# Optimization experiments

Hardware: AMD Instinct MI355X
Metric: run time of the kernel (lower is better)

The kernel has to match this reference:

```python
import jax, jax.numpy as jnp
import numpy as np


def setup_inputs() -> dict:
    key = jax.random.key(0)
    ks = jax.random.split(key, 9)
    B, T, S, E, H = 4, 4096, 4096, 512, 64
    return {
        "x": jax.random.normal(ks[0], (B, T, 1), dtype=jnp.float32),
        "tok_emb": jax.random.normal(ks[1], (B, S, E), dtype=jnp.float32),
        "key_w": jax.random.normal(ks[2], (H, E), dtype=jnp.float32) * 0.05,
        "key_b": jax.random.normal(ks[3], (H,), dtype=jnp.float32) * 0.05,
        "query_w": jax.random.normal(ks[4], (H, 1), dtype=jnp.float32) * 0.05,
        "query_b": jax.random.normal(ks[5], (H,), dtype=jnp.float32) * 0.05,
        "value_w": jax.random.normal(ks[6], (H, E), dtype=jnp.float32) * 0.05,
        "proj_w": jax.random.normal(ks[7], (1, H), dtype=jnp.float32) * 0.05,
        "proj_b": jax.random.normal(ks[8], (1,), dtype=jnp.float32) * 0.05,
    }


def reference(x, tok_emb, key_w, key_b, query_w, query_b, value_w, proj_w, proj_b):
    # k = tanh(Linear(tok_emb))            [B,S,H]
    k = jnp.tanh(jnp.einsum("bse,he->bsh", tok_emb, key_w) + key_b)
    # q = tanh(Linear(x)); x last dim is 1 [B,T,H]
    q = jnp.tanh(jnp.einsum("btu,hu->bth", x, query_w) + query_b)
    scale = k.shape[-1] ** (-0.5)
    wei = jnp.einsum("bth,bsh->bts", q, k) * scale  # [B,T,S]
    # NOTE: softmax over dim=-2 (the query/T axis), faithful to the original
    wei = jax.nn.softmax(wei, axis=-2)
    v = jnp.tanh(jnp.einsum("bse,he->bsh", tok_emb, value_w))  # [B,S,H]
    out = jnp.tanh(jnp.einsum("bts,bsh->bth", wei, v))         # [B,T,H]
    out = jnp.einsum("bth,oh->bto", out, proj_w) + proj_b      # [B,T,1]
    return jnp.squeeze(out, axis=-1)                            # [B,T]
```

## Files before the change

### kernel.cpp

```cpp
#include <hip/hip_runtime.h>
#include <math.h>

#define BB 4
#define TT 4096
#define SS 4096
#define EE 512
#define HH 64
#define NN 128
#define XR 6.0f


typedef __attribute__((ext_vector_type(8))) __bf16 bf16x8;
typedef __attribute__((ext_vector_type(16))) float f32x16;

__device__ __forceinline__ unsigned short f2b(float f) {
  unsigned int u = __float_as_uint(f);
  return (unsigned short)((u + 0x7FFFu + ((u >> 16) & 1u)) >> 16);
}

__global__ __launch_bounds__(256) void prep_sm_kernel(
    const float* __restrict__ kw, const float* __restrict__ vw,
    const float* __restrict__ qw, const float* __restrict__ qb,
    const float* __restrict__ x, unsigned int* __restrict__ Wfrag,
    float* __restrict__ Cmat, unsigned short* __restrict__ qnA,
    float* __restrict__ Sm_part) {
  const int blk = blockIdx.x;
  if (blk < 64) {
    int idx = blk * 256 + threadIdx.x;
    int jq = idx & 1;
    int l = (idx >> 1) & 63;
    int ks = (idx >> 7) & 31;
    int nb = idx >> 12;
    int n = nb * 32 + (l & 31);
    int k = ks * 16 + (l >> 5) * 8 + jq * 4;
    const float* row = (n < HH) ? (kw + n * EE + k) : (vw + (n - HH) * EE + k);
    float4 wv = *(const float4*)row;
    Wfrag[idx * 2] = (unsigned int)f2b(wv.x) | ((unsigned int)f2b(wv.y) << 16);
    Wfrag[idx * 2 + 1] =
        (unsigned int)f2b(wv.z) | ((unsigned int)f2b(wv.w) << 16);
  } else if (blk < 128) {
    int idx = (blk - 64) * 256 + threadIdx.x;
    int m = idx >> 7;
    int j = idx & (NN - 1);
    Cmat[idx] = (float)cos((double)m * (M_PI * (j + 0.5) / NN));
  } else if (blk < 160) {
    int idx = (blk - 128) * 256 + threadIdx.x;
    int h = idx & 63;
    int j = idx >> 6;
    double th = M_PI * (j + 0.5) / NN;
    float xj = (float)(XR * cos(th));
    float val = tanhf(fmaf(xj, qw[h], qb[h]));
    int pos = (((j >> 5) * 4 + (h >> 4)) * 64 + (j & 31) + 32 * ((h >> 3) & 1)) * 8 +
              (h & 7);
    qnA[pos] = f2b(val);
  } else {
    __shared__ float theta[128];
    int blk2 = blk - 160;
    int b = blk2 >> 5;
    int chunk = blk2 & 31;
    int t0 = chunk * 128;
    int tid = threadIdx.x;
    if (tid < 128) {
      float xh = x[b * TT + t0 + tid] * (1.0f / XR);
      xh = fminf(1.0f, fmaxf(-1.0f, xh));
      theta[tid] = acosf(xh);
    }
    __syncthreads();
    if (tid < 128) {
      float m = (float)tid;
      float acc = 0.f;
#pragma unroll 8
      for (int i = 0; i < 128; ++i) acc += cosf(m * theta[i]);
      Sm_part[(b * 32 + chunk) * NN + tid] = acc;
    }
  }
}

__global__ __launch_bounds__(256) void kvattn_kernel(
    const float* __restrict__ emb, const float* __restrict__ kb,
    const unsigned int* __restrict__ Wfrag, const unsigned short* __restrict__ qnA,
    const float* __restrict__ Cmat, const float* __restrict__ Sm_part,
    float* __restrict__ Opart) {
  __shared__ __align__(16) char smem[69120];
  unsigned short* A_lds = (unsigned short*)smem;
  unsigned short* ktB = (unsigned short*)smem;
  unsigned short* vB = (unsigned short*)(smem + 8192);
  unsigned short* eA = (unsigned short*)(smem + 16384);
  float* zred = (float*)(smem + 65536);
  float* wql = (float*)(smem + 67840);
  float* izl = (float*)(smem + 68352);
  float* sml = (float*)(smem + 68608);

  const int tid = threadIdx.x;
  const int row0 = blockIdx.x * 64;
  const int bb = row0 >> 12;
  const int sc = (row0 >> 6) & 63;

#pragma unroll
  for (int mb = 0; mb < 2; ++mb) {
    int m = tid >> 3;
    int c8 = tid & 7;
    const float* src = emb + (size_t)(row0 + mb * 32 + m) * EE;
    unsigned short* dst = A_lds + mb * 16384;
#pragma unroll
    for (int it = 0; it < 16; ++it) {
      int k = (c8 + it * 8) * 4;
      float4 v = *(const float4*)(src + k);
      int kstep = k >> 4;
      int lane = m + 32 * ((k >> 3) & 1);
      int j = k & 7;
      unsigned int lo = (unsigned int)f2b(v.x) | ((unsigned int)f2b(v.y) << 16);
      unsigned int hi = (unsigned int)f2b(v.z) | ((unsigned int)f2b(v.w) << 16);
      *(uint2*)&dst[(kstep * 64 + lane) * 8 + j] = make_uint2(lo, hi);
    }
  }
  if (tid < 128) {
    float s = 0.f;
#pragma unroll 8
    for (int c = 0; c < 32; ++c) s += Sm_part[(bb * 32 + c) * NN + tid];
    sml[tid] = s;
  }
  __syncthreads();
  if (tid < 128) {
    float acc = sml[0] * (1.0f / NN);
    for (int m = 1; m < NN; ++m)
      acc = fmaf(sml[m] * (2.0f / NN), Cmat[m * NN + tid], acc);
    wql[tid] = acc;
  }

  const int w = tid >> 6;
  const int lane = tid & 63;
  f32x16 acc0 = {}, acc1 = {};
  const bf16x8* Bf = (const bf16x8*)Wfrag;
#pragma unroll 4
  for (int kstep = 0; kstep < 32; ++kstep) {
    bf16x8 bfr = Bf[(w * 32 + kstep) * 64 + lane];
    bf16x8 a0 = *(const bf16x8*)&A_lds[(kstep * 64 + lane) * 8];
    bf16x8 a1 = *(const bf16x8*)&A_lds[16384 + (kstep * 64 + lane) * 8];
    acc0 = __builtin_amdgcn_mfma_f32_32x32x16_bf16(a0, bfr, acc0, 0, 0, 0);
    acc1 = __builtin_amdgcn_mfma_f32_32x32x16_bf16(a1, bfr, acc1, 0, 0, 0);
  }
  __syncthreads();

  {
    const int n = w * 32 + (lane & 31);
    if (w < 2) {
      float kbv = kb[n];
      const int ks_h = n >> 4;
      const int off_h = 32 * ((n >> 3) & 1);
      const int jj_h = n & 7;
#pragma unroll
      for (int reg = 0; reg < 16; ++reg) {
        int sl = (reg & 3) + 8 * (reg >> 2) + 4 * (lane >> 5);
        ktB[(ks_h * 64 + sl + off_h) * 8 + jj_h] = f2b(tanhf(acc0[reg] + kbv));
        ktB[((4 + ks_h) * 64 + sl + off_h) * 8 + jj_h] =
            f2b(tanhf(acc1[reg] + kbv));
      }
    } else {
      int h = n - 64;
      const int nb_h = h >> 5;
      const int lm = h & 31;
#pragma unroll
      for (int reg = 0; reg < 16; ++reg) {
        int sl = (reg & 3) + 8 * (reg >> 2) + 4 * (lane >> 5);
        int s1 = sl + 32;
        vB[((nb_h * 4 + (sl >> 4)) * 64 + lm + 32 * ((sl >> 3) & 1)) * 8 +
           (sl & 7)] = f2b(tanhf(acc0[reg]));
        vB[((nb_h * 4 + (s1 >> 4)) * 64 + lm + 32 * ((s1 >> 3) & 1)) * 8 +
           (s1 & 7)] = f2b(tanhf(acc1[reg]));
      }
    }
  }
  __syncthreads();

  f32x16 l0 = {}, l1 = {};
#pragma unroll
  for (int ks = 0; ks < 4; ++ks) {
    bf16x8 a = *(const bf16x8*)(qnA + ((w * 4 + ks) * 64 + lane) * 8);
    bf16x8 b0 = *(const bf16x8*)&ktB[(ks * 64 + lane) * 8];
    bf16x8 b1 = *(const bf16x8*)&ktB[((4 + ks) * 64 + lane) * 8];
    l0 = __builtin_amdgcn_mfma_f32_32x32x16_bf16(a, b0, l0, 0, 0, 0);
    l1 = __builtin_amdgcn_mfma_f32_32x32x16_bf16(a, b1, l1, 0, 0, 0);
  }
  float e0[16], e1[16];
  float zp0 = 0.f, zp1 = 0.f;
#pragma unroll
  for (int r = 0; r < 4; ++r) {
    float4 wq4 = *(const float4*)&wql[w * 32 + 8 * r + 4 * (lane >> 5)];
    float wa[4] = {wq4.x, wq4.y, wq4.z, wq4.w};
#pragma unroll
    for (int c = 0; c < 4; ++c) {
      int reg = 4 * r + c;
      e0[reg] = __expf(l0[reg] * 0.125f);
      e1[reg] = __expf(l1[reg] * 0.125f);
      zp0 = fmaf(wa[c], e0[reg], zp0);
      zp1 = fmaf(wa[c], e1[reg], zp1);
    }
  }
  zred[(lane & 31) * 9 + w * 2 + (lane >> 5)] = zp0;
  zred[(32 + (lane & 31)) * 9 + w * 2 + (lane >> 5)] = zp1;
  __syncthreads();
  if (tid < 64) {
    float sum = 0.f;
#pragma unroll
    for (int k = 0; k < 8; ++k) sum += zred[tid * 9 + k];
    izl[tid] = 1.0f / sum;
  }
  __syncthreads();

  {
    const int sA = lane & 31, sB = 32 + (lane & 31);
    const float izA = izl[sA], izB = izl[sB];
    const int ksA = sA >> 4, oA = 32 * ((sA >> 3) & 1), jA = sA & 7;
    const int ksB = sB >> 4, oB = 32 * ((sB >> 3) & 1), jB = sB & 7;
#pragma unroll
    for (int reg = 0; reg < 16; ++reg) {
      int jl = (reg & 3) + 8 * (reg >> 2) + 4 * (lane >> 5);
      eA[((w * 4 + ksA) * 64 + jl + oA) * 8 + jA] = f2b(e0[reg] * izA);
      eA[((w * 4 + ksB) * 64 + jl + oB) * 8 + jB] = f2b(e1[reg] * izB);
    }
  }
  __syncthreads();
  f32x16 o0 = {}, o1 = {};
#pragma unroll
  for (int ks = 0; ks < 4; ++ks) {
    bf16x8 a = *(const bf16x8*)&eA[((w * 4 + ks) * 64 + lane) * 8];
    bf16x8 b0 = *(const bf16x8*)&vB[(ks * 64 + lane) * 8];
    bf16x8 b1 = *(const bf16x8*)&vB[((4 + ks) * 64 + lane) * 8];
    o0 = __builtin_amdgcn_mfma_f32_32x32x16_bf16(a, b0, o0, 0, 0, 0);
    o1 = __builtin_amdgcn_mfma_f32_32x32x16_bf16(a, b1, o1, 0, 0, 0);
  }
  float* op = Opart + (size_t)(bb * 64 + sc) * (NN * HH);
  const int h0 = lane & 31, h1 = 32 + (lane & 31);
#pragma unroll
  for (int reg = 0; reg < 16; ++reg) {
    int j = w * 32 + (reg & 3) + 8 * (reg >> 2) + 4 * (lane >> 5);
    op[j * HH + h0] = o0[reg];
    op[j * HH + h1] = o1[reg];
  }
}

__global__ __launch_bounds__(256) void oy_kernel(const float* __restrict__ Opart,
                                                 const float* __restrict__ pw,
                                                 const float* __restrict__ pb,
                                                 float* __restrict__ ynode) {
  __shared__ float part[2][4][64];
  const int tid = threadIdx.x;
  const int b = blockIdx.x >> 6;
  const int j0 = (blockIdx.x & 63) * 2;
  const int h = tid & 63;
  const int q = tid >> 6;
#pragma unroll
  for (int jj = 0; jj < 2; ++jj) {
    float s = 0.f;
#pragma unroll
    for (int i = 0; i < 16; ++i)
      s += Opart[((size_t)(b * 64 + q * 16 + i) * NN + j0 + jj) * HH + h];
    part[jj][q][h] = s;
  }
  __syncthreads();
  if (tid < 128) {
    int jj = tid >> 6;
    int lane = tid & 63;
    float o = part[jj][0][lane] + part[jj][1][lane] + part[jj][2][lane] +
              part[jj][3][lane];
    float v = tanhf(o) * pw[lane];
#pragma unroll
    for (int off = 32; off > 0; off >>= 1) v += __shfl_down(v, off, 64);
    if (lane == 0) ynode[b * NN + j0 + jj] = v + pb[0];
  }
}

__global__ __launch_bounds__(256) void final_kernel(
    const float* __restrict__ x, const float* __restrict__ ynode,
    const float* __restrict__ Cmat, float* __restrict__ y) {
  const int idx = blockIdx.x * 256 + threadIdx.x;
  const int b = idx >> 12;
  __shared__ float yl[NN];
  __shared__ float c[NN];
  if (threadIdx.x < NN) yl[threadIdx.x] = ynode[b * NN + threadIdx.x];
  __syncthreads();
  if (threadIdx.x < NN) {
    int m = threadIdx.x;
    double acc = 0.0;
#pragma unroll 8
    for (int j = 0; j < NN; ++j)
      acc += (double)yl[j] * (double)Cmat[m * NN + j];
    c[m] = (float)(acc * ((m == 0 ? 1.0 : 2.0) / NN));
  }
  __syncthreads();
  float xf = x[idx] * (1.0f / XR);
  xf = fminf(1.0f, fmaxf(-1.0f, xf));
  double xh = (double)xf;
  double b1 = 0.0, b2 = 0.0;
  for (int m = NN - 1; m >= 1; --m) {
    double t = fma(2.0 * xh, b1, (double)c[m] - b2);
    b2 = b1;
    b1 = t;
  }
  y[idx] = (float)fma(xh, b1, (double)c[0] - b2);
}

extern "C" void kernel_launch(void* const* d_in, const int* in_sizes, int n_in,
                              void* d_out, int out_size, void* d_ws,
                              size_t ws_size, hipStream_t stream) {
  const float* x = (const float*)d_in[0];
  const float* emb = (const float*)d_in[1];
  const float* kw = (const float*)d_in[2];
  const float* kb = (const float*)d_in[3];
  const float* qw = (const float*)d_in[4];
  const float* qb = (const float*)d_in[5];
  const float* vw = (const float*)d_in[6];
  const float* pw = (const float*)d_in[7];
  const float* pb = (const float*)d_in[8];

  float* ws = (float*)d_ws;
  float* Opart = ws;
  float* Cmat = ws + (2 << 20);
  unsigned short* qnA = (unsigned short*)(Cmat + 16384);
  unsigned int* Wfrag = (unsigned int*)(Cmat + 16384 + 4096);
  float* Sm_part = (float*)(Wfrag + 32768);
  float* ynode = Sm_part + 16384;
  float* y = (float*)d_out;

  prep_sm_kernel<<<288, 256, 0, stream>>>(kw, vw, qw, qb, x, Wfrag, Cmat, qnA,
                                          Sm_part);
  kvattn_kernel<<<BB * SS / 64, 256, 0, stream>>>(emb, kb, Wfrag, qnA, Cmat,
                                                  Sm_part, Opart);
  oy_kernel<<<BB * NN / 2, 256, 0, stream>>>(Opart, pw, pb, ynode);
  final_kernel<<<BB * TT / 256, 256, 0, stream>>>(x, ynode, Cmat, y);
}
```

Baseline: 135.3 us.

## Fuse four kernels into one cooperative kernel with grid-wide syncs

Merges the prep, KV-attention, output reduction and final Chebyshev evaluation kernels into a single cooperative launch of 256 blocks separated by grid.sync barriers. This removes three kernel launch boundaries and their idle gaps. The prep work is redistributed across the 256 blocks, and the final stage now uses only 64 of 256 threads per block. Grid barriers have their own cost, and the cooperative launch requires all 256 blocks with 69KB of shared memory each to be resident at once.

```diff
diff --git a/kernel.cpp b/kernel.cpp
--- a/kernel.cpp
+++ b/kernel.cpp
@@ -1,5 +1,8 @@
 #include <hip/hip_runtime.h>
+#include <hip/hip_cooperative_groups.h>
 #include <math.h>
+
+namespace cg = cooperative_groups;
 
 #define BB 4
 #define TT 4096
@@ -18,15 +21,48 @@
   return (unsigned short)((u + 0x7FFFu + ((u >> 16) & 1u)) >> 16);
 }
 
-__global__ __launch_bounds__(256) void prep_sm_kernel(
-    const float* __restrict__ kw, const float* __restrict__ vw,
+__global__ __launch_bounds__(256) void mega_kernel(
+    const float* __restrict__ x, const float* __restrict__ emb,
+    const float* __restrict__ kw, const float* __restrict__ kb,
     const float* __restrict__ qw, const float* __restrict__ qb,
-    const float* __restrict__ x, unsigned int* __restrict__ Wfrag,
+    const float* __restrict__ vw, const float* __restrict__ pw,
+    const float* __restrict__ pb, unsigned int* __restrict__ Wfrag,
     float* __restrict__ Cmat, unsigned short* __restrict__ qnA,
-    float* __restrict__ Sm_part) {
+    float* __restrict__ Sm_part, float* __restrict__ Opart,
+    float* __restrict__ ynode, float* __restrict__ y) {
+  cg::grid_group grid = cg::this_grid();
+  __shared__ __align__(16) char smem[69120];
+  const int tid = threadIdx.x;
   const int blk = blockIdx.x;
-  if (blk < 64) {
-    int idx = blk * 256 + threadIdx.x;
+
+  if (blk < 128) {
+    float* theta = (float*)(smem + 65536);
+    int b = blk >> 5, chunk = blk & 31, t0 = chunk * 128;
+    if (tid < 128) {
+      float xh = x[b * TT + t0 + tid] * (1.0f / XR);
+      xh = fminf(1.0f, fmaxf(-1.0f, xh));
+      theta[tid] = acosf(xh);
+    }
+    __syncthreads();
+    if (tid < 128) {
+      float m = (float)tid;
+      float acc = 0.f;
+#pragma unroll 8
+      for (int i = 0; i < 128; ++i) acc += cosf(m * theta[i]);
+      Sm_part[(b * 32 + chunk) * NN + tid] = acc;
+    }
+  } else if (blk < 160) {
+    int idx = (blk - 128) * 256 + tid;
+    int h = idx & 63;
+    int j = idx >> 6;
+    double th = M_PI * (j + 0.5) / NN;
+    float xj = (float)(XR * cos(th));
+    float val = tanhf(fmaf(xj, qw[h], qb[h]));
+    int pos = (((j >> 5) * 4 + (h >> 4)) * 64 + (j & 31) + 32 * ((h >> 3) & 1)) * 8 +
+              (h & 7);
+    qnA[pos] = f2b(val);
+  } else if (blk < 224) {
+    int idx = (blk - 160) * 256 + tid;
     int jq = idx & 1;
     int l = (idx >> 1) & 63;
     int ks = (idx >> 7) & 31;
@@ -38,267 +74,237 @@
     Wfrag[idx * 2] = (unsigned int)f2b(wv.x) | ((unsigned int)f2b(wv.y) << 16);
     Wfrag[idx * 2 + 1] =
         (unsigned int)f2b(wv.z) | ((unsigned int)f2b(wv.w) << 16);
-  } else if (blk < 128) {
-    int idx = (blk - 64) * 256 + threadIdx.x;
-    int m = idx >> 7;
-    int j = idx & (NN - 1);
-    Cmat[idx] = (float)cos((double)m * (M_PI * (j + 0.5) / NN));
-  } else if (blk < 160) {
-    int idx = (blk - 128) * 256 + threadIdx.x;
-    int h = idx & 63;
-    int j = idx >> 6;
-    double th = M_PI * (j + 0.5) / NN;
-    float xj = (float)(XR * cos(th));
-    float val = tanhf(fmaf(xj, qw[h], qb[h]));
-    int pos = (((j >> 5) * 4 + (h >> 4)) * 64 + (j & 31) + 32 * ((h >> 3) & 1)) * 8 +
-              (h & 7);
-    qnA[pos] = f2b(val);
   } else {
-    __shared__ float theta[128];
-    int blk2 = blk - 160;
-    int b = blk2 >> 5;
-    int chunk = blk2 & 31;
-    int t0 = chunk * 128;
-    int tid = threadIdx.x;
-    if (tid < 128) {
-      float xh = x[b * TT + t0 + tid] * (1.0f / XR);
-      xh = fminf(1.0f, fmaxf(-1.0f, xh));
-      theta[tid] = acosf(xh);
-    }
-    __syncthreads();
-    if (tid < 128) {
-      float m = (float)tid;
-      float acc = 0.f;
+    int idx = (blk - 224) * 256 + tid;
+#pragma unroll
+    for (int r = 0; r < 2; ++r) {
+      int id2 = idx + r * 8192;
+      int m = id2 >> 7;
+      int j = id2 & (NN - 1);
+      Cmat[id2] = (float)cos((double)m * (M_PI * (j + 0.5) / NN));
+    }
+  }
+  grid.sync();
+
+  {
+    unsigned short* A_lds = (unsigned short*)smem;
+    unsigned short* ktB = (unsigned short*)smem;
+    unsigned short* vB = (unsigned short*)(smem + 8192);
+    unsigned short* eA = (unsigned short*)(smem + 16384);
+    float* zred = (float*)(smem + 65536);
+    float* wql = (float*)(smem + 67840);
+    float* izl = (float*)(smem + 68352);
+    float* sml = (float*)(smem + 68608);
+
+    const int row0 = blk * 64;
+    const int bb = row0 >> 12;
+    const int sc = (row0 >> 6) & 63;
+
+#pragma unroll
+    for (int mb = 0; mb < 2; ++mb) {
+      int m = tid >> 3;
+      int c8 = tid & 7;
+      const float* src = emb + (size_t)(row0 + mb * 32 + m) * EE;
+      unsigned short* dst = A_lds + mb * 16384;
+#pragma unroll
+      for (int it = 0; it < 16; ++it) {
+        int k = (c8 + it * 8) * 4;
+        float4 v = *(const float4*)(src + k);
+        int kstep = k >> 4;
+        int lane = m + 32 * ((k >> 3) & 1);
+        int j = k & 7;
+        unsigned int lo =
+            (unsigned int)f2b(v.x) | ((unsigned int)f2b(v.y) << 16);
+        unsigned int hi =
+            (unsigned int)f2b(v.z) | ((unsigned int)f2b(v.w) << 16);
+        *(uint2*)&dst[(kstep * 64 + lane) * 8 + j] = make_uint2(lo, hi);
+      }
+    }
+    if (tid < 128) {
+      float s = 0.f;
 #pragma unroll 8
-      for (int i = 0; i < 128; ++i) acc += cosf(m * theta[i]);
-      Sm_part[(b * 32 + chunk) * NN + tid] = acc;
+      for (int c = 0; c < 32; ++c) s += Sm_part[(bb * 32 + c) * NN + tid];
+      sml[tid] = s;
+    }
+    __syncthreads();
+    if (tid < 128) {
+      float acc = sml[0] * (1.0f / NN);
+      for (int m = 1; m < NN; ++m)
+        acc = fmaf(sml[m] * (2.0f / NN), Cmat[m * NN + tid], acc);
+      wql[tid] = acc;
+    }
+
+    const int w = tid >> 6;
+    const int lane = tid & 63;
+    f32x16 acc0 = {}, acc1 = {};
+    const bf16x8* Bf = (const bf16x8*)Wfrag;
+#pragma unroll 4
+    for (int kstep = 0; kstep < 32; ++kstep) {
+      bf16x8 bfr = Bf[(w * 32 + kstep) * 64 + lane];
+      bf16x8 a0 = *(const bf16x8*)&A_lds[(kstep * 64 + lane) * 8];
+      bf16x8 a1 = *(const bf16x8*)&A_lds[16384 + (kstep * 64 + lane) * 8];
+      acc0 = __builtin_amdgcn_mfma_f32_32x32x16_bf16(a0, bfr, acc0, 0, 0, 0);
+      acc1 = __builtin_amdgcn_mfma_f32_32x32x16_bf16(a1, bfr, acc1, 0, 0, 0);
+    }
+    __syncthreads();
+
+    {
+      const int n = w * 32 + (lane & 31);
+      if (w < 2) {
+        float kbv = kb[n];
+        const int ks_h = n >> 4;
+        const int off_h = 32 * ((n >> 3) & 1);
+        const int jj_h = n & 7;
+#pragma unroll
+        for (int reg = 0; reg < 16; ++reg) {
+          int sl = (reg & 3) + 8 * (reg >> 2) + 4 * (lane >> 5);
+          ktB[(ks_h * 64 + sl + off_h) * 8 + jj_h] =
+              f2b(tanhf(acc0[reg] + kbv));
+          ktB[((4 + ks_h) * 64 + sl + off_h) * 8 + jj_h] =
+              f2b(tanhf(acc1[reg] + kbv));
+        }
+      } else {
+        int h = n - 64;
+        const int nb_h = h >> 5;
+        const int lm = h & 31;
+#pragma unroll
+        for (int reg = 0; reg < 16; ++reg) {
+          int sl = (reg & 3) + 8 * (reg >> 2) + 4 * (lane >> 5);
+          int s1 = sl + 32;
+          vB[((nb_h * 4 + (sl >> 4)) * 64 + lm + 32 * ((sl >> 3) & 1)) * 8 +
+             (sl & 7)] = f2b(tanhf(acc0[reg]));
+          vB[((nb_h * 4 + (s1 >> 4)) * 64 + lm + 32 * ((s1 >> 3) & 1)) * 8 +
+             (s1 & 7)] = f2b(tanhf(acc1[reg]));
+        }
+      }
+    }
+    __syncthreads();
+
+    f32x16 l0 = {}, l1 = {};
+#pragma unroll
+    for (int ks = 0; ks < 4; ++ks) {
+      bf16x8 a = *(const bf16x8*)(qnA + ((w * 4 + ks) * 64 + lane) * 8);
+      bf16x8 b0 = *(const bf16x8*)&ktB[(ks * 64 + lane) * 8];
+      bf16x8 b1 = *(const bf16x8*)&ktB[((4 + ks) * 64 + lane) * 8];
+      l0 = __builtin_amdgcn_mfma_f32_32x32x16_bf16(a, b0, l0, 0, 0, 0);
+      l1 = __builtin_amdgcn_mfma_f32_32x32x16_bf16(a, b1, l1, 0, 0, 0);
+    }
+    float e0[16], e1[16];
+    float zp0 = 0.f, zp1 = 0.f;
+#pragma unroll
+    for (int r = 0; r < 4; ++r) {
+      float4 wq4 = *(const float4*)&wql[w * 32 + 8 * r + 4 * (lane >> 5)];
+      float wa[4] = {wq4.x, wq4.y, wq4.z, wq4.w};
+#pragma unroll
+      for (int c = 0; c < 4; ++c) {
+        int reg = 4 * r + c;
+        e0[reg] = __expf(l0[reg] * 0.125f);
+        e1[reg] = __expf(l1[reg] * 0.125f);
+        zp0 = fmaf(wa[c], e0[reg], zp0);
+        zp1 = fmaf(wa[c], e1[reg], zp1);
+      }
+    }
+    zred[(lane & 31) * 9 + w * 2 + (lane >> 5)] = zp0;
+    zred[(32 + (lane & 31)) * 9 + w * 2 + (lane >> 5)] = zp1;
+    __syncthreads();
+    if (tid < 64) {
+      float sum = 0.f;
+#pragma unroll
+      for (int k = 0; k < 8; ++k) sum += zred[tid * 9 + k];
+      izl[tid] = 1.0f / sum;
+    }
+    __syncthreads();
+
+    {
+      const int sA = lane & 31, sB = 32 + (lane & 31);
+      const float izA = izl[sA], izB = izl[sB];
+      const int ksA = sA >> 4, oA = 32 * ((sA >> 3) & 1), jA = sA & 7;
+      const int ksB = sB >> 4, oB = 32 * ((sB >> 3) & 1), jB = sB & 7;
+#pragma unroll
+      for (int reg = 0; reg < 16; ++reg) {
+        int jl = (reg & 3) + 8 * (reg >> 2) + 4 * (lane >> 5);
+        eA[((w * 4 + ksA) * 64 + jl + oA) * 8 + jA] = f2b(e0[reg] * izA);
+        eA[((w * 4 + ksB) * 64 + jl + oB) * 8 + jB] = f2b(e1[reg] * izB);
+      }
+    }
+    __syncthreads();
+    f32x16 o0 = {}, o1 = {};
+#pragma unroll
+    for (int ks = 0; ks < 4; ++ks) {
+      bf16x8 a = *(const bf16x8*)&eA[((w * 4 + ks) * 64 + lane) * 8];
+      bf16x8 b0 = *(const bf16x8*)&vB[(ks * 64 + lane) * 8];
+      bf16x8 b1 = *(const bf16x8*)&vB[((4 + ks) * 64 + lane) * 8];
+      o0 = __builtin_amdgcn_mfma_f32_32x32x16_bf16(a, b0, o0, 0, 0, 0);
+      o1 = __builtin_amdgcn_mfma_f32_32x32x16_bf16(a, b1, o1, 0, 0, 0);
+    }
+    float* op = Opart + (size_t)(bb * 64 + sc) * (NN * HH);
+    const int h0 = lane & 31, h1 = 32 + (lane & 31);
+#pragma unroll
+    for (int reg = 0; reg < 16; ++reg) {
+      int j = w * 32 + (reg & 3) + 8 * (reg >> 2) + 4 * (lane >> 5);
+      op[j * HH + h0] = o0[reg];
+      op[j * HH + h1] = o1[reg];
     }
   }
-}
-
-__global__ __launch_bounds__(256) void kvattn_kernel(
-    const float* __restrict__ emb, const float* __restrict__ kb,
-    const unsigned int* __restrict__ Wfrag, const unsigned short* __restrict__ qnA,
-    const float* __restrict__ Cmat, const float* __restrict__ Sm_part,
-    float* __restrict__ Opart) {
-  __shared__ __align__(16) char smem[69120];
-  unsigned short* A_lds = (unsigned short*)smem;
-  unsigned short* ktB = (unsigned short*)smem;
-  unsigned short* vB = (unsigned short*)(smem + 8192);
-  unsigned short* eA = (unsigned short*)(smem + 16384);
-  float* zred = (float*)(smem + 65536);
-  float* wql = (float*)(smem + 67840);
-  float* izl = (float*)(smem + 68352);
-  float* sml = (float*)(smem + 68608);
-
-  const int tid = threadIdx.x;
-  const int row0 = blockIdx.x * 64;
-  const int bb = row0 >> 12;
-  const int sc = (row0 >> 6) & 63;
-
-#pragma unroll
-  for (int mb = 0; mb < 2; ++mb) {
-    int m = tid >> 3;
-    int c8 = tid & 7;
-    const float* src = emb + (size_t)(row0 + mb * 32 + m) * EE;
-    unsigned short* dst = A_lds + mb * 16384;
-#pragma unroll
-    for (int it = 0; it < 16; ++it) {
-      int k = (c8 + it * 8) * 4;
-      float4 v = *(const float4*)(src + k);
-      int kstep = k >> 4;
-      int lane = m + 32 * ((k >> 3) & 1);
-      int j = k & 7;
-      unsigned int lo = (unsigned int)f2b(v.x) | ((unsigned int)f2b(v.y) << 16);
-      unsigned int hi = (unsigned int)f2b(v.z) | ((unsigned int)f2b(v.w) << 16);
-      *(uint2*)&dst[(kstep * 64 + lane) * 8 + j] = make_uint2(lo, hi);
+  grid.sync();
+
+  {
+    float (*part)[4][64] = (float(*)[4][64])smem;
+    const int b = blk >> 6;
+    const int j0 = (blk & 63) * 2;
+    const int h = tid & 63;
+    const int q = tid >> 6;
+#pragma unroll
+    for (int jj = 0; jj < 2; ++jj) {
+      float s = 0.f;
+#pragma unroll
+      for (int i = 0; i < 16; ++i)
+        s += Opart[((size_t)(b * 64 + q * 16 + i) * NN + j0 + jj) * HH + h];
+      part[jj][q][h] = s;
+    }
+    __syncthreads();
+    if (tid < 128) {
+      int jj = tid >> 6;
+      int lane = tid & 63;
+      float o = part[jj][0][lane] + part[jj][1][lane] + part[jj][2][lane] +
+                part[jj][3][lane];
+      float v = tanhf(o) * pw[lane];
+#pragma unroll
+      for (int off = 32; off > 0; off >>= 1) v += __shfl_down(v, off, 64);
+      if (lane == 0) ynode[b * NN + j0 + jj] = v + pb[0];
     }
   }
-  if (tid < 128) {
-    float s = 0.f;
+  grid.sync();
+
+  {
+    float* yl = (float*)smem;
+    float* c = (float*)(smem + 512);
+    const int base = blk * 64;
+    const int b = base >> 12;
+    if (tid < NN) yl[tid] = ynode[b * NN + tid];
+    __syncthreads();
+    if (tid < NN) {
+      double acc = 0.0;
 #pragma unroll 8
-    for (int c = 0; c < 32; ++c) s += Sm_part[(bb * 32 + c) * NN + tid];
-    sml[tid] = s;
+      for (int j = 0; j < NN; ++j)
+        acc += (double)yl[j] * (double)Cmat[tid * NN + j];
+      c[tid] = (float)(acc * ((tid == 0 ? 1.0 : 2.0) / NN));
+    }
+    __syncthreads();
+    if (tid < 64) {
+      const int idx = base + tid;
+      float xf = x[idx] * (1.0f / XR);
+      xf = fminf(1.0f, fmaxf(-1.0f, xf));
+      double xh = (double)xf;
+      double b1 = 0.0, b2 = 0.0;
+      for (int m = NN - 1; m >= 1; --m) {
+        double t = fma(2.0 * xh, b1, (double)c[m] - b2);
+        b2 = b1;
+        b1 = t;
+      }
+      y[idx] = (float)fma(xh, b1, (double)c[0] - b2);
+    }
   }
-  __syncthreads();
-  if (tid < 128) {
-    float acc = sml[0] * (1.0f / NN);
-    for (int m = 1; m < NN; ++m)
-      acc = fmaf(sml[m] * (2.0f / NN), Cmat[m * NN + tid], acc);
-    wql[tid] = acc;
-  }
-
-  const int w = tid >> 6;
-  const int lane = tid & 63;
-  f32x16 acc0 = {}, acc1 = {};
-  const bf16x8* Bf = (const bf16x8*)Wfrag;
-#pragma unroll 4
-  for (int kstep = 0; kstep < 32; ++kstep) {
-    bf16x8 bfr = Bf[(w * 32 + kstep) * 64 + lane];
-    bf16x8 a0 = *(const bf16x8*)&A_lds[(kstep * 64 + lane) * 8];
-    bf16x8 a1 = *(const bf16x8*)&A_lds[16384 + (kstep * 64 + lane) * 8];
-    acc0 = __builtin_amdgcn_mfma_f32_32x32x16_bf16(a0, bfr, acc0, 0, 0, 0);
-    acc1 = __builtin_amdgcn_mfma_f32_32x32x16_bf16(a1, bfr, acc1, 0, 0, 0);
-  }
-  __syncthreads();
-
-  {
-    const int n = w * 32 + (lane & 31);
-    if (w < 2) {
-      float kbv = kb[n];
-      const int ks_h = n >> 4;
-      const int off_h = 32 * ((n >> 3) & 1);
-      const int jj_h = n & 7;
-#pragma unroll
-      for (int reg = 0; reg < 16; ++reg) {
-        int sl = (reg & 3) + 8 * (reg >> 2) + 4 * (lane >> 5);
-        ktB[(ks_h * 64 + sl + off_h) * 8 + jj_h] = f2b(tanhf(acc0[reg] + kbv));
-        ktB[((4 + ks_h) * 64 + sl + off_h) * 8 + jj_h] =
-            f2b(tanhf(acc1[reg] + kbv));
-      }
-    } else {
-      int h = n - 64;
-      const int nb_h = h >> 5;
-      const int lm = h & 31;
-#pragma unroll
-      for (int reg = 0; reg < 16; ++reg) {
-        int sl = (reg & 3) + 8 * (reg >> 2) + 4 * (lane >> 5);
-        int s1 = sl + 32;
-        vB[((nb_h * 4 + (sl >> 4)) * 64 + lm + 32 * ((sl >> 3) & 1)) * 8 +
-           (sl & 7)] = f2b(tanhf(acc0[reg]));
-        vB[((nb_h * 4 + (s1 >> 4)) * 64 + lm + 32 * ((s1 >> 3) & 1)) * 8 +
-           (s1 & 7)] = f2b(tanhf(acc1[reg]));
-      }
-    }
-  }
-  __syncthreads();
-
-  f32x16 l0 = {}, l1 = {};
-#pragma unroll
-  for (int ks = 0; ks < 4; ++ks) {
-    bf16x8 a = *(const bf16x8*)(qnA + ((w * 4 + ks) * 64 + lane) * 8);
-    bf16x8 b0 = *(const bf16x8*)&ktB[(ks * 64 + lane) * 8];
-    bf16x8 b1 = *(const bf16x8*)&ktB[((4 + ks) * 64 + lane) * 8];
-    l0 = __builtin_amdgcn_mfma_f32_32x32x16_bf16(a, b0, l0, 0, 0, 0);
-    l1 = __builtin_amdgcn_mfma_f32_32x32x16_bf16(a, b1, l1, 0, 0, 0);
-  }
-  float e0[16], e1[16];
-  float zp0 = 0.f, zp1 = 0.f;
-#pragma unroll
-  for (int r = 0; r < 4; ++r) {
-    float4 wq4 = *(const float4*)&wql[w * 32 + 8 * r + 4 * (lane >> 5)];
-    float wa[4] = {wq4.x, wq4.y, wq4.z, wq4.w};
-#pragma unroll
-    for (int c = 0; c < 4; ++c) {
-      int reg = 4 * r + c;
-      e0[reg] = __expf(l0[reg] * 0.125f);
-      e1[reg] = __expf(l1[reg] * 0.125f);
-      zp0 = fmaf(wa[c], e0[reg], zp0);
-      zp1 = fmaf(wa[c], e1[reg], zp1);
-    }
-  }
-  zred[(lane & 31) * 9 + w * 2 + (lane >> 5)] = zp0;
-  zred[(32 + (lane & 31)) * 9 + w * 2 + (lane >> 5)] = zp1;
-  __syncthreads();
-  if (tid < 64) {
-    float sum = 0.f;
-#pragma unroll
-    for (int k = 0; k < 8; ++k) sum += zred[tid * 9 + k];
-    izl[tid] = 1.0f / sum;
-  }
-  __syncthreads();
-
-  {
-    const int sA = lane & 31, sB = 32 + (lane & 31);
-    const float izA = izl[sA], izB = izl[sB];
-    const int ksA = sA >> 4, oA = 32 * ((sA >> 3) & 1), jA = sA & 7;
-    const int ksB = sB >> 4, oB = 32 * ((sB >> 3) & 1), jB = sB & 7;
-#pragma unroll
-    for (int reg = 0; reg < 16; ++reg) {
-      int jl = (reg & 3) + 8 * (reg >> 2) + 4 * (lane >> 5);
-      eA[((w * 4 + ksA) * 64 + jl + oA) * 8 + jA] = f2b(e0[reg] * izA);
-      eA[((w * 4 + ksB) * 64 + jl + oB) * 8 + jB] = f2b(e1[reg] * izB);
-    }
-  }
-  __syncthreads();
-  f32x16 o0 = {}, o1 = {};
-#pragma unroll
-  for (int ks = 0; ks < 4; ++ks) {
-    bf16x8 a = *(const bf16x8*)&eA[((w * 4 + ks) * 64 + lane) * 8];
-    bf16x8 b0 = *(const bf16x8*)&vB[(ks * 64 + lane) * 8];
-    bf16x8 b1 = *(const bf16x8*)&vB[((4 + ks) * 64 + lane) * 8];
-    o0 = __builtin_amdgcn_mfma_f32_32x32x16_bf16(a, b0, o0, 0, 0, 0);
-    o1 = __builtin_amdgcn_mfma_f32_32x32x16_bf16(a, b1, o1, 0, 0, 0);
-  }
-  float* op = Opart + (size_t)(bb * 64 + sc) * (NN * HH);
-  const int h0 = lane & 31, h1 = 32 + (lane & 31);
-#pragma unroll
-  for (int reg = 0; reg < 16; ++reg) {
-    int j = w * 32 + (reg & 3) + 8 * (reg >> 2) + 4 * (lane >> 5);
-    op[j * HH + h0] = o0[reg];
-    op[j * HH + h1] = o1[reg];
-  }
-}
-
-__global__ __launch_bounds__(256) void oy_kernel(const float* __restrict__ Opart,
-                                                 const float* __restrict__ pw,
-                                                 const float* __restrict__ pb,
-                                                 float* __restrict__ ynode) {
-  __shared__ float part[2][4][64];
-  const int tid = threadIdx.x;
-  const int b = blockIdx.x >> 6;
-  const int j0 = (blockIdx.x & 63) * 2;
-  const int h = tid & 63;
-  const int q = tid >> 6;
-#pragma unroll
-  for (int jj = 0; jj < 2; ++jj) {
-    float s = 0.f;
-#pragma unroll
-    for (int i = 0; i < 16; ++i)
-      s += Opart[((size_t)(b * 64 + q * 16 + i) * NN + j0 + jj) * HH + h];
-    part[jj][q][h] = s;
-  }
-  __syncthreads();
-  if (tid < 128) {
-    int jj = tid >> 6;
-    int lane = tid & 63;
-    float o = part[jj][0][lane] + part[jj][1][lane] + part[jj][2][lane] +
-              part[jj][3][lane];
-    float v = tanhf(o) * pw[lane];
-#pragma unroll
-    for (int off = 32; off > 0; off >>= 1) v += __shfl_down(v, off, 64);
-    if (lane == 0) ynode[b * NN + j0 + jj] = v + pb[0];
-  }
-}
-
-__global__ __launch_bounds__(256) void final_kernel(
-    const float* __restrict__ x, const float* __restrict__ ynode,
-    const float* __restrict__ Cmat, float* __restrict__ y) {
-  const int idx = blockIdx.x * 256 + threadIdx.x;
-  const int b = idx >> 12;
-  __shared__ float yl[NN];
-  __shared__ float c[NN];
-  if (threadIdx.x < NN) yl[threadIdx.x] = ynode[b * NN + threadIdx.x];
-  __syncthreads();
-  if (threadIdx.x < NN) {
-    int m = threadIdx.x;
-    double acc = 0.0;
-#pragma unroll 8
-    for (int j = 0; j < NN; ++j)
-      acc += (double)yl[j] * (double)Cmat[m * NN + j];
-    c[m] = (float)(acc * ((m == 0 ? 1.0 : 2.0) / NN));
-  }
-  __syncthreads();
-  float xf = x[idx] * (1.0f / XR);
-  xf = fminf(1.0f, fmaxf(-1.0f, xf));
-  double xh = (double)xf;
-  double b1 = 0.0, b2 = 0.0;
-  for (int m = NN - 1; m >= 1; --m) {
-    double t = fma(2.0 * xh, b1, (double)c[m] - b2);
-    b2 = b1;
-    b1 = t;
-  }
-  y[idx] = (float)fma(xh, b1, (double)c[0] - b2);
 }
 
 extern "C" void kernel_launch(void* const* d_in, const int* in_sizes, int n_in,
@@ -323,10 +329,9 @@
   float* ynode = Sm_part + 16384;
   float* y = (float*)d_out;
 
-  prep_sm_kernel<<<288, 256, 0, stream>>>(kw, vw, qw, qb, x, Wfrag, Cmat, qnA,
-                                          Sm_part);
-  kvattn_kernel<<<BB * SS / 64, 256, 0, stream>>>(emb, kb, Wfrag, qnA, Cmat,
-                                                  Sm_part, Opart);
-  oy_kernel<<<BB * NN / 2, 256, 0, stream>>>(Opart, pw, pb, ynode);
-  final_kernel<<<BB * TT / 256, 256, 0, stream>>>(x, ynode, Cmat, y);
+  void* args[] = {&x,  &emb,   &kw,   &kb,      &qw,    &qb,
+                  &vw, &pw,    &pb,   &Wfrag,   &Cmat,  &qnA,
+                  &Sm_part, &Opart, &ynode, &y};
+  hipLaunchCooperativeKernel((void*)mega_kernel, dim3(256), dim3(256), args, 0,
+                             stream);
 }
```

Result: slower. 230.1 us (+70.1%).

## Stage embedding tile in two halves to halve LDS footprint

Applied to the files above, without the earlier changes.

The 64-row embedding tile is now converted to bf16 and staged in LDS one 32-row half at a time, with the MFMA loop split into two passes that reuse a single 32 KB buffer. This cuts the kernel's shared memory from about 69 KB to about 36 KB so more blocks can be resident per CU. In exchange the Wfrag fragments are loaded twice, extra barriers are added, and the second half's global load is serialized behind the first half's compute within a block.

```diff
diff --git a/kernel.cpp b/kernel.cpp
--- a/kernel.cpp
+++ b/kernel.cpp
@@ -81,37 +81,38 @@
     const unsigned int* __restrict__ Wfrag, const unsigned short* __restrict__ qnA,
     const float* __restrict__ Cmat, const float* __restrict__ Sm_part,
     float* __restrict__ Opart) {
-  __shared__ __align__(16) char smem[69120];
-  unsigned short* A_lds = (unsigned short*)smem;
+  __shared__ __align__(16) char smem[36352];
+  unsigned short* A_half = (unsigned short*)smem;
   unsigned short* ktB = (unsigned short*)smem;
   unsigned short* vB = (unsigned short*)(smem + 8192);
   unsigned short* eA = (unsigned short*)(smem + 16384);
-  float* zred = (float*)(smem + 65536);
-  float* wql = (float*)(smem + 67840);
-  float* izl = (float*)(smem + 68352);
-  float* sml = (float*)(smem + 68608);
+  float* zred = (float*)(smem + 32768);
+  float* wql = (float*)(smem + 35072);
+  float* izl = (float*)(smem + 35584);
+  float* sml = (float*)(smem + 35840);
 
   const int tid = threadIdx.x;
   const int row0 = blockIdx.x * 64;
   const int bb = row0 >> 12;
   const int sc = (row0 >> 6) & 63;
-
-#pragma unroll
-  for (int mb = 0; mb < 2; ++mb) {
+  const int w = tid >> 6;
+  const int lane = tid & 63;
+  const bf16x8* Bf = (const bf16x8*)Wfrag;
+
+  {
     int m = tid >> 3;
     int c8 = tid & 7;
-    const float* src = emb + (size_t)(row0 + mb * 32 + m) * EE;
-    unsigned short* dst = A_lds + mb * 16384;
+    const float* src = emb + (size_t)(row0 + m) * EE;
 #pragma unroll
     for (int it = 0; it < 16; ++it) {
       int k = (c8 + it * 8) * 4;
       float4 v = *(const float4*)(src + k);
       int kstep = k >> 4;
-      int lane = m + 32 * ((k >> 3) & 1);
+      int l = m + 32 * ((k >> 3) & 1);
       int j = k & 7;
       unsigned int lo = (unsigned int)f2b(v.x) | ((unsigned int)f2b(v.y) << 16);
       unsigned int hi = (unsigned int)f2b(v.z) | ((unsigned int)f2b(v.w) << 16);
-      *(uint2*)&dst[(kstep * 64 + lane) * 8 + j] = make_uint2(lo, hi);
+      *(uint2*)&A_half[(kstep * 64 + l) * 8 + j] = make_uint2(lo, hi);
     }
   }
   if (tid < 128) {
@@ -128,16 +129,35 @@
     wql[tid] = acc;
   }
 
-  const int w = tid >> 6;
-  const int lane = tid & 63;
   f32x16 acc0 = {}, acc1 = {};
-  const bf16x8* Bf = (const bf16x8*)Wfrag;
 #pragma unroll 4
   for (int kstep = 0; kstep < 32; ++kstep) {
     bf16x8 bfr = Bf[(w * 32 + kstep) * 64 + lane];
-    bf16x8 a0 = *(const bf16x8*)&A_lds[(kstep * 64 + lane) * 8];
-    bf16x8 a1 = *(const bf16x8*)&A_lds[16384 + (kstep * 64 + lane) * 8];
+    bf16x8 a0 = *(const bf16x8*)&A_half[(kstep * 64 + lane) * 8];
     acc0 = __builtin_amdgcn_mfma_f32_32x32x16_bf16(a0, bfr, acc0, 0, 0, 0);
+  }
+  __syncthreads();
+  {
+    int m = tid >> 3;
+    int c8 = tid & 7;
+    const float* src = emb + (size_t)(row0 + 32 + m) * EE;
+#pragma unroll
+    for (int it = 0; it < 16; ++it) {
+      int k = (c8 + it * 8) * 4;
+      float4 v = *(const float4*)(src + k);
+      int kstep = k >> 4;
+      int l = m + 32 * ((k >> 3) & 1);
+      int j = k & 7;
+      unsigned int lo = (unsigned int)f2b(v.x) | ((unsigned int)f2b(v.y) << 16);
+      unsigned int hi = (unsigned int)f2b(v.z) | ((unsigned int)f2b(v.w) << 16);
+      *(uint2*)&A_half[(kstep * 64 + l) * 8 + j] = make_uint2(lo, hi);
+    }
+  }
+  __syncthreads();
+#pragma unroll 4
+  for (int kstep = 0; kstep < 32; ++kstep) {
+    bf16x8 bfr = Bf[(w * 32 + kstep) * 64 + lane];
+    bf16x8 a1 = *(const bf16x8*)&A_half[(kstep * 64 + lane) * 8];
     acc1 = __builtin_amdgcn_mfma_f32_32x32x16_bf16(a1, bfr, acc1, 0, 0, 0);
   }
   __syncthreads();
```

New measurement: 138.0 us. About the same (+2.0%).
